# Kernel tuning notes

Hardware: AMD Instinct MI355X
Metric: run time of the kernel (lower is better)

Reference implementation:

```python
import jax, jax.numpy as jnp
import numpy as np

N = 100000      # nodes
E = 1600000     # edges (avg degree 16)
D = 64          # in_channels == conv widths == lin width
G = 64          # graphs in batch
OUT = 10        # out_channels


def setup_inputs() -> dict:
    key = jax.random.key(0)
    ks = jax.random.split(key, 20)
    s = 0.1
    inp = {
        "x": jax.random.normal(ks[0], (N, D), jnp.float32),
        "edge_index": jax.random.randint(ks[1], (2, E), 0, N, dtype=jnp.int64),
        "batch": jnp.sort(jax.random.randint(ks[2], (N,), 0, G, dtype=jnp.int64)),
    }
    k = 3
    for i in range(3):  # 3 SAGEConv layers: lin_l (Wl, bl) on aggregated, lin_r (Wr, no bias) on root
        inp[f"c{i}_Wl"] = jax.random.normal(ks[k], (D, D), jnp.float32) * s; k += 1
        inp[f"c{i}_bl"] = jnp.zeros((D,), jnp.float32)
        inp[f"c{i}_Wr"] = jax.random.normal(ks[k], (D, D), jnp.float32) * s; k += 1
    inp["l0_W"] = jax.random.normal(ks[k], (D, D), jnp.float32) * s; k += 1
    inp["l0_b"] = jnp.zeros((D,), jnp.float32)
    inp["out_W"] = jax.random.normal(ks[k], (D, OUT), jnp.float32) * s; k += 1
    inp["out_b"] = jnp.zeros((OUT,), jnp.float32)
    return inp


def reference(x, edge_index, batch,
              c0_Wl, c0_bl, c0_Wr,
              c1_Wl, c1_bl, c1_Wr,
              c2_Wl, c2_bl, c2_Wr,
              l0_W, l0_b, out_W, out_b):
    src, dst = edge_index[0], edge_index[1]
    # in-degree of each target node (mean conv aggregation), computed once
    deg = jax.ops.segment_sum(jnp.ones((E,), x.dtype), dst, num_segments=N)
    inv_deg = (1.0 / jnp.maximum(deg, 1.0))[:, None]

    def sage(h, Wl, bl, Wr):
        # gather source features, mean-aggregate at targets, then lin_l(agg) + lin_r(h)
        agg = jax.ops.segment_sum(h[src], dst, num_segments=N) * inv_deg
        return agg @ Wl + bl + h @ Wr

    h = jax.nn.relu(sage(x, c0_Wl, c0_bl, c0_Wr))
    h = jax.nn.relu(sage(h, c1_Wl, c1_bl, c1_Wr))
    h = jax.nn.relu(sage(h, c2_Wl, c2_bl, c2_Wr))

    # global mean pool over graphs
    cnt = jax.ops.segment_sum(jnp.ones((N,), h.dtype), batch, num_segments=G)
    g = jax.ops.segment_sum(h, batch, num_segments=G) / jnp.maximum(cnt, 1.0)[:, None]

    g = jax.nn.relu(g @ l0_W + l0_b)
    return g @ out_W + out_b  # [G, OUT]
```

## Files before the change

### kernel.cpp

```cpp
#include <hip/hip_runtime.h>
#include <hip/hip_fp16.h>

#define WPB 8
#define PADK 136
#define BSH 8
#define BNODES 256
#define SC_BLOCKS 256
#define HIST_BLOCKS 256
#define HSTRIDE 512

typedef _Float16 half8 __attribute__((ext_vector_type(8)));
typedef _Float16 half4v __attribute__((ext_vector_type(4)));
typedef float floatx4 __attribute__((ext_vector_type(4)));

__global__ __launch_bounds__(256) void gnn_pre(const int* __restrict__ dst,
                                               int* __restrict__ bkt_cnt, int nbkt, int E,
                                               const int* __restrict__ batch,
                                               float* __restrict__ gcnt, int N,
                                               const float4* __restrict__ xin,
                                               ushort4* __restrict__ x16o, int n4,
                                               __half* __restrict__ x16,
                                               __half* __restrict__ hA,
                                               __half* __restrict__ hB,
                                               int* __restrict__ hist_all) {
    int tid = threadIdx.x;
    if (blockIdx.x < HIST_BLOCKS) {
        __shared__ int h[512];
        __shared__ int gb[64];
        for (int i = tid; i < nbkt; i += 256) h[i] = 0;
        if (tid < 64) gb[tid] = 0;
        __syncthreads();
        const int stride = HIST_BLOCKS * 256;
        if ((E & 3) == 0) {
            const int4* dst4 = (const int4*)dst;
            int E4 = E >> 2;
            for (int e = blockIdx.x * 256 + tid; e < E4; e += stride) {
                int4 d = dst4[e];
                atomicAdd(&h[d.x >> BSH], 1);
                atomicAdd(&h[d.y >> BSH], 1);
                atomicAdd(&h[d.z >> BSH], 1);
                atomicAdd(&h[d.w >> BSH], 1);
            }
        } else {
            for (int e = blockIdx.x * 256 + tid; e < E; e += stride)
                atomicAdd(&h[dst[e] >> BSH], 1);
        }
        for (int i = blockIdx.x * 256 + tid; i < N; i += stride)
            atomicAdd(&gb[batch[i]], 1);
        __syncthreads();
        for (int i = tid; i < nbkt; i += 256) {
            int v = h[i];
            hist_all[blockIdx.x * HSTRIDE + i] = v;
            if (v) atomicAdd(&bkt_cnt[i], v);
        }
        if (tid < 64) {
            int v = gb[tid];
            if (v) atomicAdd(&gcnt[tid], (float)v);
        }
        if (blockIdx.x == 0 && tid < 64) {
            x16[(size_t)N * 64 + tid] = __ushort_as_half((unsigned short)0);
            hA[(size_t)N * 64 + tid] = __ushort_as_half((unsigned short)0);
            hB[(size_t)N * 64 + tid] = __ushort_as_half((unsigned short)0);
        }
    } else {
        int i = (blockIdx.x - HIST_BLOCKS) * 256 + tid;
        if (i < n4) {
            float4 f = xin[i];
            ushort4 o;
            o.x = __half_as_ushort(__float2half(f.x));
            o.y = __half_as_ushort(__float2half(f.y));
            o.z = __half_as_ushort(__float2half(f.z));
            o.w = __half_as_ushort(__float2half(f.w));
            x16o[i] = o;
        }
    }
}

__global__ void gnn_bkt_scan(const int* __restrict__ bkt_cnt, int* __restrict__ bkt_base,
                             int* __restrict__ row_ptr, int nbkt, int N) {
    int lane = threadIdx.x;
    int carry = 0;
    for (int base = 0; base < nbkt; base += 64) {
        int idx = base + lane;
        int v = (idx < nbkt) ? bkt_cnt[idx] : 0;
        int x = v;
#pragma unroll
        for (int off = 1; off < 64; off <<= 1) {
            int y = __shfl_up(x, off);
            if (lane >= off) x += y;
        }
        if (idx < nbkt) bkt_base[idx] = carry + (x - v);
        carry += __shfl(x, 63);
    }
    if (lane == 0) {
        bkt_base[nbkt] = carry;
        row_ptr[N] = carry;
    }
}

__global__ __launch_bounds__(256) void gnn_scan2(const int* __restrict__ hist_all,
                                                 const int* __restrict__ bkt_base,
                                                 int* __restrict__ blk_base_all, int nbkt) {
    int b = blockIdx.x;
    int t = threadIdx.x, lane = t & 63, wv = t >> 6;
    __shared__ int wsum[4];
    int v = hist_all[t * HSTRIDE + b];
    int x = v;
#pragma unroll
    for (int off = 1; off < 64; off <<= 1) {
        int y = __shfl_up(x, off);
        if (lane >= off) x += y;
    }
    if (lane == 63) wsum[wv] = x;
    __syncthreads();
    int wexcl = 0;
    for (int w = 0; w < wv; w++) wexcl += wsum[w];
    blk_base_all[t * HSTRIDE + b] = bkt_base[b] + wexcl + (x - v);
}

__global__ __launch_bounds__(256) void gnn_bkt_scatter(const int* __restrict__ src,
                                                       const int* __restrict__ dst,
                                                       const int* __restrict__ blk_base_all,
                                                       unsigned int* __restrict__ pairs,
                                                       int E, int nbkt) {
    __shared__ int cur[512];
    int tid = threadIdx.x;
    for (int i = tid; i < nbkt; i += 256) cur[i] = blk_base_all[blockIdx.x * HSTRIDE + i];
    __syncthreads();
    const int stride = SC_BLOCKS * 256;
    if ((E & 3) == 0) {
        const int4* dst4 = (const int4*)dst;
        const int4* src4 = (const int4*)src;
        int E4 = E >> 2;
        for (int e = blockIdx.x * 256 + tid; e < E4; e += stride) {
            int4 d = dst4[e];
            int4 s = src4[e];
            int p0 = atomicAdd(&cur[d.x >> BSH], 1);
            pairs[p0] = (unsigned int)s.x | ((unsigned int)(d.x & (BNODES - 1)) << 24);
            int p1 = atomicAdd(&cur[d.y >> BSH], 1);
            pairs[p1] = (unsigned int)s.y | ((unsigned int)(d.y & (BNODES - 1)) << 24);
            int p2 = atomicAdd(&cur[d.z >> BSH], 1);
            pairs[p2] = (unsigned int)s.z | ((unsigned int)(d.z & (BNODES - 1)) << 24);
            int p3 = atomicAdd(&cur[d.w >> BSH], 1);
            pairs[p3] = (unsigned int)s.w | ((unsigned int)(d.w & (BNODES - 1)) << 24);
        }
    } else {
        for (int e = blockIdx.x * 256 + tid; e < E; e += stride) {
            int d = dst[e];
            int b = d >> BSH;
            int p = atomicAdd(&cur[b], 1);
            pairs[p] = (unsigned int)src[e] | ((unsigned int)(d & (BNODES - 1)) << 24);
        }
    }
}

__global__ __launch_bounds__(256) void gnn_bkt_csr(const unsigned int* __restrict__ pairs,
                                                   const int* __restrict__ bkt_base,
                                                   int* __restrict__ row_ptr,
                                                   float* __restrict__ inv_deg,
                                                   int* __restrict__ csr_src, int N) {
    __shared__ int hist[BNODES];
    __shared__ int excl[BNODES];
    __shared__ int cur[BNODES];
    int b = blockIdx.x;
    int base = bkt_base[b];
    int cnt = bkt_base[b + 1] - base;
    int nd0 = b << BSH;
    int tid = threadIdx.x;
    hist[tid] = 0;
    __syncthreads();
    {
        int a0 = (4 - (base & 3)) & 3;
        a0 = min(a0, cnt);
        for (int i = tid; i < a0; i += 256) atomicAdd(&hist[pairs[base + i] >> 24], 1);
        int vcnt = (cnt - a0) >> 2;
        const uint4* p4 = (const uint4*)(pairs + base + a0);
        for (int i = tid; i < vcnt; i += 256) {
            uint4 u = p4[i];
            atomicAdd(&hist[u.x >> 24], 1);
            atomicAdd(&hist[u.y >> 24], 1);
            atomicAdd(&hist[u.z >> 24], 1);
            atomicAdd(&hist[u.w >> 24], 1);
        }
        for (int i = a0 + (vcnt << 2) + tid; i < cnt; i += 256)
            atomicAdd(&hist[pairs[base + i] >> 24], 1);
    }
    __syncthreads();
    if (tid < 64) {
        int carry = 0;
#pragma unroll
        for (int c = 0; c < BNODES; c += 64) {
            int v = hist[c + tid];
            int x = v;
#pragma unroll
            for (int off = 1; off < 64; off <<= 1) {
                int y = __shfl_up(x, off);
                if (tid >= off) x += y;
            }
            excl[c + tid] = carry + (x - v);
            carry += __shfl(x, 63);
        }
    }
    __syncthreads();
    {
        int node = nd0 + tid;
        if (node < N) {
            row_ptr[node] = base + excl[tid];
            int d = hist[tid];
            inv_deg[node] = 1.0f / (float)(d > 1 ? d : 1);
        }
        cur[tid] = excl[tid];
    }
    __syncthreads();
    {
        int a0 = (4 - (base & 3)) & 3;
        a0 = min(a0, cnt);
        for (int i = tid; i < a0; i += 256) {
            unsigned int u = pairs[base + i];
            int pos = atomicAdd(&cur[u >> 24], 1);
            csr_src[base + pos] = (int)(u & 0xFFFFFFu);
        }
        int vcnt = (cnt - a0) >> 2;
        const uint4* p4 = (const uint4*)(pairs + base + a0);
        for (int i = tid; i < vcnt; i += 256) {
            uint4 u = p4[i];
            int pos0 = atomicAdd(&cur[u.x >> 24], 1);
            csr_src[base + pos0] = (int)(u.x & 0xFFFFFFu);
            int pos1 = atomicAdd(&cur[u.y >> 24], 1);
            csr_src[base + pos1] = (int)(u.y & 0xFFFFFFu);
            int pos2 = atomicAdd(&cur[u.z >> 24], 1);
            csr_src[base + pos2] = (int)(u.z & 0xFFFFFFu);
            int pos3 = atomicAdd(&cur[u.w >> 24], 1);
            csr_src[base + pos3] = (int)(u.w & 0xFFFFFFu);
        }
        for (int i = a0 + (vcnt << 2) + tid; i < cnt; i += 256) {
            unsigned int u = pairs[base + i];
            int pos = atomicAdd(&cur[u >> 24], 1);
            csr_src[base + pos] = (int)(u & 0xFFFFFFu);
        }
    }
}

#define LOAD4(eReg, c0, vArr)                                  \
    _Pragma("unroll") for (int c_ = 0; c_ < 4; c_++) {         \
        int sj_ = __shfl(eReg, (c0) + c_ * 4 + quad);          \
        vArr[c_] = hin4v[(size_t)sj_ * 16 + m16];              \
    }
#define ACC4(vArr, accum)                                      \
    _Pragma("unroll") for (int c_ = 0; c_ < 4; c_++) {         \
        accum.x += (float)vArr[c_][0];                         \
        accum.y += (float)vArr[c_][1];                         \
        accum.z += (float)vArr[c_][2];                         \
        accum.w += (float)vArr[c_][3];                         \
    }

__global__ __launch_bounds__(512, 4) void gnn_sage(const __half* __restrict__ hin,
                                                   __half* __restrict__ hout,
                                                   const int* __restrict__ row_ptr,
                                                   const int* __restrict__ csr_src,
                                                   const float* __restrict__ inv_deg,
                                                   const float* __restrict__ Wl,
                                                   const float* __restrict__ bl,
                                                   const float* __restrict__ Wr, int n) {
    __shared__ _Float16 w_lds[64 * PADK];
    __shared__ _Float16 in_lds[WPB][16 * PADK];
    int tid = threadIdx.x, lane = tid & 63, wv = tid >> 6;
    for (int i = tid; i < 64 * 64; i += 512) {
        int k = i >> 6, nn = i & 63;
        w_lds[nn * PADK + k] = (_Float16)Wl[i];
        w_lds[nn * PADK + 64 + k] = (_Float16)Wr[i];
    }
    __syncthreads();
    int ngroups = (n + 15) >> 4;
    int g = blockIdx.x * WPB + wv;
    if (g >= ngroups) return;
    int m16 = lane & 15, quad = lane >> 4;
    int hf = lane >> 5, col = lane & 31;
    float bias[4];
#pragma unroll
    for (int nt = 0; nt < 4; nt++) bias[nt] = bl[nt * 16 + m16];
    _Float16* my_in = in_lds[wv];
    const unsigned* hin32 = (const unsigned*)hin;
    const half4v* hin4v = (const half4v*)hin;
    int nd0 = g << 4;
    int nclamp = n - 1 - nd0;
    int idx = nd0 + lane;
    int rr = (lane <= 16) ? row_ptr[min(idx, n)] : 0;
    float ig = (lane < 16) ? inv_deg[min(idx, n - 1)] : 0.0f;

#pragma unroll
    for (int jp = 0; jp < 8; jp++) {
        int j2 = jp << 1;
        int nd = nd0 + min(j2 + hf, nclamp);
        unsigned u = hin32[(size_t)nd * 32 + col];
        ((unsigned*)(my_in + (j2 + hf) * PADK + 64))[col] = u;
    }

    int ef[16];
#pragma unroll
    for (int j = 0; j < 16; j++) {
        int jj = min(j, nclamp);
        int s0 = __shfl(rr, jj), s1 = __shfl(rr, jj + 1);
        int cb = min(64, s1 - s0);
        ef[j] = (lane < cb) ? csr_src[s0 + lane] : n;
    }

#pragma unroll
    for (int jp = 0; jp < 8; jp++) {
        int j2 = jp << 1;
        int jjA = min(j2, nclamp), jjB = min(j2 + 1, nclamp);
        int s0A = __shfl(rr, jjA), s1A = __shfl(rr, jjA + 1);
        int s0B = __shfl(rr, jjB), s1B = __shfl(rr, jjB + 1);
        float idgA = __shfl(ig, jjA), idgB = __shfl(ig, jjB);
        int cbA = min(64, s1A - s0A), cbB = min(64, s1B - s0B);
        floatx4 accA = {0.f, 0.f, 0.f, 0.f};
        floatx4 accB = {0.f, 0.f, 0.f, 0.f};
        {
            half4v vA[4], vB[4];
            LOAD4(ef[j2], 0, vA);
            LOAD4(ef[j2 + 1], 0, vB);
            ACC4(vA, accA);
            ACC4(vB, accB);
        }
        if (cbA > 16) {
            half4v v0[4];
            LOAD4(ef[j2], 16, v0);
            ACC4(v0, accA);
            if (cbA > 32) { half4v v1[4]; LOAD4(ef[j2], 32, v1); ACC4(v1, accA); }
            if (cbA > 48) { half4v v2[4]; LOAD4(ef[j2], 48, v2); ACC4(v2, accA); }
        }
        if (cbB > 16) {
            half4v v0[4];
            LOAD4(ef[j2 + 1], 16, v0);
            ACC4(v0, accB);
            if (cbB > 32) { half4v v1[4]; LOAD4(ef[j2 + 1], 32, v1); ACC4(v1, accB); }
            if (cbB > 48) { half4v v2[4]; LOAD4(ef[j2 + 1], 48, v2); ACC4(v2, accB); }
        }
        for (int base_ = s0A + 64; base_ < s1A; base_ += 64) {
            int cb = min(64, s1A - base_);
            int ei = (lane < cb) ? csr_src[base_ + lane] : n;
            for (int i0 = 0; i0 < cb; i0 += 16) {
                half4v vt[4];
                LOAD4(ei, i0, vt);
                ACC4(vt, accA);
            }
        }
        for (int base_ = s0B + 64; base_ < s1B; base_ += 64) {
            int cb = min(64, s1B - base_);
            int ei = (lane < cb) ? csr_src[base_ + lane] : n;
            for (int i0 = 0; i0 < cb; i0 += 16) {
                half4v vt[4];
                LOAD4(ei, i0, vt);
                ACC4(vt, accB);
            }
        }
        accA.x += __shfl_xor(accA.x, 16); accA.y += __shfl_xor(accA.y, 16);
        accA.z += __shfl_xor(accA.z, 16); accA.w += __shfl_xor(accA.w, 16);
        accA.x += __shfl_xor(accA.x, 32); accA.y += __shfl_xor(accA.y, 32);
        accA.z += __shfl_xor(accA.z, 32); accA.w += __shfl_xor(accA.w, 32);
        accB.x += __shfl_xor(accB.x, 16); accB.y += __shfl_xor(accB.y, 16);
        accB.z += __shfl_xor(accB.z, 16); accB.w += __shfl_xor(accB.w, 16);
        accB.x += __shfl_xor(accB.x, 32); accB.y += __shfl_xor(accB.y, 32);
        accB.z += __shfl_xor(accB.z, 32); accB.w += __shfl_xor(accB.w, 32);
        if (quad == 0) {
            half4v hw;
            hw[0] = (_Float16)(accA.x * idgA);
            hw[1] = (_Float16)(accA.y * idgA);
            hw[2] = (_Float16)(accA.z * idgA);
            hw[3] = (_Float16)(accA.w * idgA);
            *(half4v*)(my_in + j2 * PADK + m16 * 4) = hw;
        } else if (quad == 1) {
            half4v hw;
            hw[0] = (_Float16)(accB.x * idgB);
            hw[1] = (_Float16)(accB.y * idgB);
            hw[2] = (_Float16)(accB.z * idgB);
            hw[3] = (_Float16)(accB.w * idgB);
            *(half4v*)(my_in + (j2 + 1) * PADK + m16 * 4) = hw;
        }
    }
    half8 afrag[4];
    const _Float16* abase = my_in + m16 * PADK + quad * 8;
#pragma unroll
    for (int ks = 0; ks < 4; ks++) afrag[ks] = *(const half8*)(abase + ks * 32);
    floatx4 accv[4];
#pragma unroll
    for (int nt = 0; nt < 4; nt++) {
        accv[nt].x = 0.f; accv[nt].y = 0.f; accv[nt].z = 0.f; accv[nt].w = 0.f;
    }
#pragma unroll
    for (int nt = 0; nt < 4; nt++) {
        const _Float16* bbase = w_lds + (nt * 16 + m16) * PADK + quad * 8;
#pragma unroll
        for (int ks = 0; ks < 4; ks++) {
            half8 bfrag = *(const half8*)(bbase + ks * 32);
            accv[nt] = __builtin_amdgcn_mfma_f32_16x16x32_f16(afrag[ks], bfrag, accv[nt], 0, 0, 0);
        }
    }
#pragma unroll
    for (int nt = 0; nt < 4; nt++) {
#pragma unroll
        for (int r = 0; r < 4; r++) {
            int node = nd0 + quad * 4 + r;
            if (node < n) {
                float v = fmaxf(accv[nt][r] + bias[nt], 0.0f);
                hout[(size_t)node * 64 + nt * 16 + m16] = __float2half(v);
            }
        }
    }
}

__global__ __launch_bounds__(512, 4) void gnn_sage_pool(const __half* __restrict__ hin,
                                                        const int* __restrict__ row_ptr,
                                                        const int* __restrict__ csr_src,
                                                        const float* __restrict__ inv_deg,
                                                        const float* __restrict__ Wl,
                                                        const float* __restrict__ bl,
                                                        const float* __restrict__ Wr,
                                                        const int* __restrict__ batch,
                                                        float* __restrict__ gsum, int n) {
    __shared__ _Float16 w_lds[64 * PADK];
    __shared__ _Float16 in_lds[WPB][16 * PADK];
    int tid = threadIdx.x, lane = tid & 63, wv = tid >> 6;
    for (int i = tid; i < 64 * 64; i += 512) {
        int k = i >> 6, nn = i & 63;
        w_lds[nn * PADK + k] = (_Float16)Wl[i];
        w_lds[nn * PADK + 64 + k] = (_Float16)Wr[i];
    }
    __syncthreads();
    int ngroups = (n + 15) >> 4;
    int g = blockIdx.x * WPB + wv;
    if (g >= ngroups) return;
    int m16 = lane & 15, quad = lane >> 4;
    int hf = lane >> 5, col = lane & 31;
    float bias[4];
#pragma unroll
    for (int nt = 0; nt < 4; nt++) bias[nt] = bl[nt * 16 + m16];
    _Float16* my_in = in_lds[wv];
    const unsigned* hin32 = (const unsigned*)hin;
    const half4v* hin4v = (const half4v*)hin;
    int nd0 = g << 4;
    int nclamp = n - 1 - nd0;
    int idx = nd0 + lane;
    int rr = (lane <= 16) ? row_ptr[min(idx, n)] : 0;
    float ig = (lane < 16) ? inv_deg[min(idx, n - 1)] : 0.0f;

#pragma unroll
    for (int jp = 0; jp < 8; jp++) {
        int j2 = jp << 1;
        int nd = nd0 + min(j2 + hf, nclamp);
        unsigned u = hin32[(size_t)nd * 32 + col];
        ((unsigned*)(my_in + (j2 + hf) * PADK + 64))[col] = u;
    }

    int ef[16];
#pragma unroll
    for (int j = 0; j < 16; j++) {
        int jj = min(j, nclamp);
        int s0 = __shfl(rr, jj), s1 = __shfl(rr, jj + 1);
        int cb = min(64, s1 - s0);
        ef[j] = (lane < cb) ? csr_src[s0 + lane] : n;
    }

#pragma unroll
    for (int jp = 0; jp < 8; jp++) {
        int j2 = jp << 1;
        int jjA = min(j2, nclamp), jjB = min(j2 + 1, nclamp);
        int s0A = __shfl(rr, jjA), s1A = __shfl(rr, jjA + 1);
        int s0B = __shfl(rr, jjB), s1B = __shfl(rr, jjB + 1);
        float idgA = __shfl(ig, jjA), idgB = __shfl(ig, jjB);
        int cbA = min(64, s1A - s0A), cbB = min(64, s1B - s0B);
        floatx4 accA = {0.f, 0.f, 0.f, 0.f};
        floatx4 accB = {0.f, 0.f, 0.f, 0.f};
        {
            half4v vA[4], vB[4];
            LOAD4(ef[j2], 0, vA);
            LOAD4(ef[j2 + 1], 0, vB);
            ACC4(vA, accA);
            ACC4(vB, accB);
        }
        if (cbA > 16) {
            half4v v0[4];
            LOAD4(ef[j2], 16, v0);
            ACC4(v0, accA);
            if (cbA > 32) { half4v v1[4]; LOAD4(ef[j2], 32, v1); ACC4(v1, accA); }
            if (cbA > 48) { half4v v2[4]; LOAD4(ef[j2], 48, v2); ACC4(v2, accA); }
        }
        if (cbB > 16) {
            half4v v0[4];
            LOAD4(ef[j2 + 1], 16, v0);
            ACC4(v0, accB);
            if (cbB > 32) { half4v v1[4]; LOAD4(ef[j2 + 1], 32, v1); ACC4(v1, accB); }
            if (cbB > 48) { half4v v2[4]; LOAD4(ef[j2 + 1], 48, v2); ACC4(v2, accB); }
        }
        for (int base_ = s0A + 64; base_ < s1A; base_ += 64) {
            int cb = min(64, s1A - base_);
            int ei = (lane < cb) ? csr_src[base_ + lane] : n;
            for (int i0 = 0; i0 < cb; i0 += 16) {
                half4v vt[4];
                LOAD4(ei, i0, vt);
                ACC4(vt, accA);
            }
        }
        for (int base_ = s0B + 64; base_ < s1B; base_ += 64) {
            int cb = min(64, s1B - base_);
            int ei = (lane < cb) ? csr_src[base_ + lane] : n;
            for (int i0 = 0; i0 < cb; i0 += 16) {
                half4v vt[4];
                LOAD4(ei, i0, vt);
                ACC4(vt, accB);
            }
        }
        accA.x += __shfl_xor(accA.x, 16); accA.y += __shfl_xor(accA.y, 16);
        accA.z += __shfl_xor(accA.z, 16); accA.w += __shfl_xor(accA.w, 16);
        accA.x += __shfl_xor(accA.x, 32); accA.y += __shfl_xor(accA.y, 32);
        accA.z += __shfl_xor(accA.z, 32); accA.w += __shfl_xor(accA.w, 32);
        accB.x += __shfl_xor(accB.x, 16); accB.y += __shfl_xor(accB.y, 16);
        accB.z += __shfl_xor(accB.z, 16); accB.w += __shfl_xor(accB.w, 16);
        accB.x += __shfl_xor(accB.x, 32); accB.y += __shfl_xor(accB.y, 32);
        accB.z += __shfl_xor(accB.z, 32); accB.w += __shfl_xor(accB.w, 32);
        if (quad == 0) {
            half4v hw;
            hw[0] = (_Float16)(accA.x * idgA);
            hw[1] = (_Float16)(accA.y * idgA);
            hw[2] = (_Float16)(accA.z * idgA);
            hw[3] = (_Float16)(accA.w * idgA);
            *(half4v*)(my_in + j2 * PADK + m16 * 4) = hw;
        } else if (quad == 1) {
            half4v hw;
            hw[0] = (_Float16)(accB.x * idgB);
            hw[1] = (_Float16)(accB.y * idgB);
            hw[2] = (_Float16)(accB.z * idgB);
            hw[3] = (_Float16)(accB.w * idgB);
            *(half4v*)(my_in + (j2 + 1) * PADK + m16 * 4) = hw;
        }
    }
    half8 afrag[4];
    const _Float16* abase = my_in + m16 * PADK + quad * 8;
#pragma unroll
    for (int ks = 0; ks < 4; ks++) afrag[ks] = *(const half8*)(abase + ks * 32);
    floatx4 accv[4];
#pragma unroll
    for (int nt = 0; nt < 4; nt++) {
        accv[nt].x = 0.f; accv[nt].y = 0.f; accv[nt].z = 0.f; accv[nt].w = 0.f;
    }
#pragma unroll
    for (int nt = 0; nt < 4; nt++) {
        const _Float16* bbase = w_lds + (nt * 16 + m16) * PADK + quad * 8;
#pragma unroll
        for (int ks = 0; ks < 4; ks++) {
            half8 bfrag = *(const half8*)(bbase + ks * 32);
            accv[nt] = __builtin_amdgcn_mfma_f32_16x16x32_f16(afrag[ks], bfrag, accv[nt], 0, 0, 0);
        }
    }
    int bFirst = batch[nd0];
    int bLast = batch[min(nd0 + 15, n - 1)];
    if (bFirst == bLast && nd0 + 15 < n) {
#pragma unroll
        for (int nt = 0; nt < 4; nt++) {
            float s = fmaxf(accv[nt][0] + bias[nt], 0.0f) + fmaxf(accv[nt][1] + bias[nt], 0.0f) +
                      fmaxf(accv[nt][2] + bias[nt], 0.0f) + fmaxf(accv[nt][3] + bias[nt], 0.0f);
            s += __shfl_xor(s, 16);
            s += __shfl_xor(s, 32);
            if (quad == 0) atomicAdd(&gsum[bFirst * 64 + nt * 16 + m16], s);
        }
    } else {
#pragma unroll
        for (int nt = 0; nt < 4; nt++) {
#pragma unroll
            for (int r = 0; r < 4; r++) {
                int node = nd0 + quad * 4 + r;
                if (node < n) {
                    int bg = batch[node];
                    float v = fmaxf(accv[nt][r] + bias[nt], 0.0f);
                    atomicAdd(&gsum[bg * 64 + nt * 16 + m16], v);
                }
            }
        }
    }
}

__global__ __launch_bounds__(1024) void gnn_head(const float* __restrict__ gsum,
                                                 const float* __restrict__ gcnt,
                                                 const float* __restrict__ l0W,
                                                 const float* __restrict__ l0b,
                                                 const float* __restrict__ outW,
                                                 const float* __restrict__ outb,
                                                 float* __restrict__ out, int G, int OUT) {
    __shared__ float gm[64 * 64];
    __shared__ float t2[64 * 64];
    int tid = threadIdx.x;
    for (int i = tid; i < G * 64; i += 1024) {
        int r = i >> 6;
        gm[i] = gsum[i] / fmaxf(gcnt[r], 1.0f);
    }
    __syncthreads();
    for (int i = tid; i < G * 64; i += 1024) {
        int r = i >> 6, c = i & 63;
        float s = l0b[c];
#pragma unroll 8
        for (int k = 0; k < 64; k++) s += gm[(r << 6) + k] * l0W[(k << 6) + c];
        t2[i] = fmaxf(s, 0.0f);
    }
    __syncthreads();
    for (int i = tid; i < G * OUT; i += 1024) {
        int r = i / OUT, c = i - r * OUT;
        float s = outb[c];
#pragma unroll 8
        for (int k = 0; k < 64; k++) s += t2[(r << 6) + k] * outW[k * OUT + c];
        out[i] = s;
    }
}

extern "C" void kernel_launch(void* const* d_in, const int* in_sizes, int n_in,
                              void* d_out, int out_size, void* d_ws, size_t ws_size,
                              hipStream_t stream) {
    const float* x = (const float*)d_in[0];
    const int* ei = (const int*)d_in[1];
    const int* batch = (const int*)d_in[2];
    const float* Wl[3] = {(const float*)d_in[3], (const float*)d_in[6], (const float*)d_in[9]};
    const float* bl[3] = {(const float*)d_in[4], (const float*)d_in[7], (const float*)d_in[10]};
    const float* Wr[3] = {(const float*)d_in[5], (const float*)d_in[8], (const float*)d_in[11]};
    const float* l0W = (const float*)d_in[12];
    const float* l0b = (const float*)d_in[13];
    const float* outW = (const float*)d_in[14];
    const float* outb = (const float*)d_in[15];

    int N = in_sizes[2];
    int E = in_sizes[1] / 2;
    int OUT = 10;
    int G = out_size / OUT;
    const int* src = ei;
    const int* dst = ei + E;
    int NBKT = (N + BNODES - 1) >> BSH;

    char* ws = (char*)d_ws;
    size_t off = 0;
    auto alloc = [&](size_t b) -> char* {
        char* p = ws + off;
        off = (off + b + 255) & ~(size_t)255;
        return p;
    };
    int* row_ptr = (int*)alloc((size_t)(N + 1) * 4);
    int* csr_src = (int*)alloc((size_t)E * 4);
    float* inv_deg = (float*)alloc((size_t)N * 4);
    size_t zoff = off;
    int* bkt_cnt = (int*)alloc((size_t)NBKT * 4);
    float* gcnt = (float*)alloc((size_t)G * 4);
    float* gsum = (float*)alloc((size_t)G * 64 * 4);
    size_t zlen = off - zoff;
    int* bkt_base = (int*)alloc((size_t)(NBKT + 1) * 4);
    int* hist_all = (int*)alloc((size_t)HIST_BLOCKS * HSTRIDE * 4);
    int* blk_base_all = (int*)alloc((size_t)HIST_BLOCKS * HSTRIDE * 4);
    unsigned int* pairs = (unsigned int*)alloc((size_t)E * 4);
    __half* x16 = (__half*)alloc((size_t)(N + 1) * 64 * 2);
    __half* hA = (__half*)alloc((size_t)(N + 1) * 64 * 2);
    __half* hB = (__half*)alloc((size_t)(N + 1) * 64 * 2);

    hipMemsetAsync(ws + zoff, 0, zlen, stream);

    int n4 = N * 64 / 4;
    int pre_blocks = HIST_BLOCKS + (n4 + 255) / 256;
    gnn_pre<<<pre_blocks, 256, 0, stream>>>(dst, bkt_cnt, NBKT, E, batch, gcnt, N,
                                            (const float4*)x, (ushort4*)x16, n4,
                                            x16, hA, hB, hist_all);
    gnn_bkt_scan<<<1, 64, 0, stream>>>(bkt_cnt, bkt_base, row_ptr, NBKT, N);
    gnn_scan2<<<NBKT, 256, 0, stream>>>(hist_all, bkt_base, blk_base_all, NBKT);
    gnn_bkt_scatter<<<SC_BLOCKS, 256, 0, stream>>>(src, dst, blk_base_all, pairs, E, NBKT);
    gnn_bkt_csr<<<NBKT, 256, 0, stream>>>(pairs, bkt_base, row_ptr, inv_deg, csr_src, N);

    int ngroups = (N + 15) >> 4;
    int sage_blocks = (ngroups + WPB - 1) / WPB;
    gnn_sage<<<sage_blocks, 512, 0, stream>>>(x16, hA, row_ptr, csr_src, inv_deg,
                                              Wl[0], bl[0], Wr[0], N);
    gnn_sage<<<sage_blocks, 512, 0, stream>>>(hA, hB, row_ptr, csr_src, inv_deg,
                                              Wl[1], bl[1], Wr[1], N);
    gnn_sage_pool<<<sage_blocks, 512, 0, stream>>>(hB, row_ptr, csr_src, inv_deg,
                                                   Wl[2], bl[2], Wr[2], batch, gsum, N);

    gnn_head<<<1, 1024, 0, stream>>>(gsum, gcnt, l0W, l0b, outW, outb, (float*)d_out, G, OUT);
}
```

Before: 293.5 us.

## Split neighbor gather across two waves per 16-node tile before MFMA

Each 16-node tile's mean-aggregation gather is now split across two waves of 8 nodes each, instead of one wave handling all 16. A block barrier follows, and then half the waves run the MFMA projection and write the output (or do the pooling atomics). The first 32 edges per node are now loaded unconditionally, and the launch bounds ask for higher occupancy. The aim is more concurrent memory-latency hiding in the irregular gather, at the cost of an extra __syncthreads, idle waves during the MFMA phase, and tighter register limits.

```diff
diff --git a/kernel.cpp b/kernel.cpp
--- a/kernel.cpp
+++ b/kernel.cpp
@@ -2,6 +2,7 @@
 #include <hip/hip_fp16.h>
 
 #define WPB 8
+#define TPB 4
 #define PADK 136
 #define BSH 8
 #define BNODES 256
@@ -254,7 +255,101 @@
         accum.w += (float)vArr[c_][3];                         \
     }
 
-__global__ __launch_bounds__(512, 4) void gnn_sage(const __half* __restrict__ hin,
+#define SAGE_GATHER_BODY                                                        \
+    int idxl = r0 + lane;                                                       \
+    int rr = (lane <= 8) ? row_ptr[min(idxl, n)] : 0;                           \
+    float ig = (lane < 8) ? inv_deg[min(idxl, n - 1)] : 0.0f;                   \
+    _Pragma("unroll")                                                           \
+    for (int jp = 0; jp < 4; jp++) {         \
+        int j2 = jp << 1;                                                       \
+        int nd = min(r0 + j2 + hf, n);                                          \
+        unsigned u = hin32[(size_t)nd * 32 + col];                              \
+        ((unsigned*)(my_in + (lr0 + j2 + hf) * PADK + 64))[col] = u;            \
+    }                                                                           \
+    int ef[8];                                                                  \
+    _Pragma("unroll")                                                           \
+    for (int j = 0; j < 8; j++) {                                               \
+        int s0 = __shfl(rr, j), s1 = __shfl(rr, j + 1);                         \
+        int cb = min(64, s1 - s0);                                              \
+        ef[j] = (lane < cb) ? csr_src[s0 + lane] : n;                           \
+    }                                                                           \
+    _Pragma("unroll")                                                           \
+    for (int jp = 0; jp < 4; jp++) {                                            \
+        int j2 = jp << 1;                                                       \
+        int s0A = __shfl(rr, j2), s1A = __shfl(rr, j2 + 1);                     \
+        int s1B = __shfl(rr, j2 + 2);                                           \
+        int s0B = s1A;                                                          \
+        float idgA = __shfl(ig, j2), idgB = __shfl(ig, j2 + 1);                 \
+        int cbA = min(64, s1A - s0A), cbB = min(64, s1B - s0B);                 \
+        floatx4 accA = {0.f, 0.f, 0.f, 0.f};                                    \
+        floatx4 accB = {0.f, 0.f, 0.f, 0.f};                                    \
+        {                                                                       \
+            half4v vA[4], vB[4];                                                \
+            LOAD4(ef[j2], 0, vA);                                               \
+            LOAD4(ef[j2 + 1], 0, vB);                                           \
+            ACC4(vA, accA);                                                     \
+            ACC4(vB, accB);                                                     \
+            LOAD4(ef[j2], 16, vA);                    \
+            LOAD4(ef[j2 + 1], 16, vB);                                          \
+            ACC4(vA, accA);                                                     \
+            ACC4(vB, accB);                                                     \
+        }                                                                       \
+        if (cbA > 32) {                                           \
+            half4v v0[4];                                                       \
+            LOAD4(ef[j2], 32, v0);                                              \
+            ACC4(v0, accA);                                                     \
+            if (cbA > 48) { half4v v1[4]; LOAD4(ef[j2], 48, v1); ACC4(v1, accA); } \
+        }                                                                       \
+        if (cbB > 32) {                                                         \
+            half4v v0[4];                                                       \
+            LOAD4(ef[j2 + 1], 32, v0);                                          \
+            ACC4(v0, accB);                                                     \
+            if (cbB > 48) { half4v v1[4]; LOAD4(ef[j2 + 1], 48, v1); ACC4(v1, accB); } \
+        }                                                                       \
+        for (int base_ = s0A + 64; base_ < s1A; base_ += 64) {                  \
+            int cb = min(64, s1A - base_);                                      \
+            int ei = (lane < cb) ? csr_src[base_ + lane] : n;                   \
+            for (int i0 = 0; i0 < cb; i0 += 16) {                               \
+                half4v vt[4];                                                   \
+                LOAD4(ei, i0, vt);                                              \
+                ACC4(vt, accA);                                                 \
+            }                                                                   \
+        }                                                                       \
+        for (int base_ = s0B + 64; base_ < s1B; base_ += 64) {                  \
+            int cb = min(64, s1B - base_);                                      \
+            int ei = (lane < cb) ? csr_src[base_ + lane] : n;                   \
+            for (int i0 = 0; i0 < cb; i0 += 16) {                               \
+                half4v vt[4];                                                   \
+                LOAD4(ei, i0, vt);                                              \
+                ACC4(vt, accB);                                                 \
+            }                                                                   \
+        }                                                                       \
+        accA.x += __shfl_xor(accA.x, 16); accA.y += __shfl_xor(accA.y, 16);     \
+        accA.z += __shfl_xor(accA.z, 16); accA.w += __shfl_xor(accA.w, 16);     \
+        accA.x += __shfl_xor(accA.x, 32); accA.y += __shfl_xor(accA.y, 32);     \
+        accA.z += __shfl_xor(accA.z, 32); accA.w += __shfl_xor(accA.w, 32);     \
+        accB.x += __shfl_xor(accB.x, 16); accB.y += __shfl_xor(accB.y, 16);     \
+        accB.z += __shfl_xor(accB.z, 16); accB.w += __shfl_xor(accB.w, 16);     \
+        accB.x += __shfl_xor(accB.x, 32); accB.y += __shfl_xor(accB.y, 32);     \
+        accB.z += __shfl_xor(accB.z, 32); accB.w += __shfl_xor(accB.w, 32);     \
+        if (quad == 0) {                                                        \
+            half4v hw;                                                          \
+            hw[0] = (_Float16)(accA.x * idgA);                                  \
+            hw[1] = (_Float16)(accA.y * idgA);                                  \
+            hw[2] = (_Float16)(accA.z * idgA);                                  \
+            hw[3] = (_Float16)(accA.w * idgA);                                  \
+            *(half4v*)(my_in + (lr0 + j2) * PADK + m16 * 4) = hw;               \
+        } else if (quad == 1) {                                                 \
+            half4v hw;                                                          \
+            hw[0] = (_Float16)(accB.x * idgB);                                  \
+            hw[1] = (_Float16)(accB.y * idgB);                                  \
+            hw[2] = (_Float16)(accB.z * idgB);                                  \
+            hw[3] = (_Float16)(accB.w * idgB);                                  \
+            *(half4v*)(my_in + (lr0 + j2 + 1) * PADK + m16 * 4) = hw;           \
+        }                                                                       \
+    }
+
+__global__ __launch_bounds__(512, 8) void gnn_sage(const __half* __restrict__ hin,
                                                    __half* __restrict__ hout,
                                                    const int* __restrict__ row_ptr,
                                                    const int* __restrict__ csr_src,
@@ -263,8 +358,8 @@
                                                    const float* __restrict__ bl,
                                                    const float* __restrict__ Wr, int n) {
     __shared__ _Float16 w_lds[64 * PADK];
-    __shared__ _Float16 in_lds[WPB][16 * PADK];
-    int tid = threadIdx.x, lane = tid & 63, wv = tid >> 6;
+    __shared__ _Float16 in_lds[TPB][16 * PADK];
+    int tid = threadIdx.x, lane = tid & 63, wvid = tid >> 6;
     for (int i = tid; i < 64 * 64; i += 512) {
         int k = i >> 6, nn = i & 63;
         w_lds[nn * PADK + k] = (_Float16)Wl[i];
@@ -272,144 +367,62 @@
     }
     __syncthreads();
     int ngroups = (n + 15) >> 4;
-    int g = blockIdx.x * WPB + wv;
-    if (g >= ngroups) return;
     int m16 = lane & 15, quad = lane >> 4;
     int hf = lane >> 5, col = lane & 31;
-    float bias[4];
-#pragma unroll
-    for (int nt = 0; nt < 4; nt++) bias[nt] = bl[nt * 16 + m16];
-    _Float16* my_in = in_lds[wv];
     const unsigned* hin32 = (const unsigned*)hin;
     const half4v* hin4v = (const half4v*)hin;
-    int nd0 = g << 4;
-    int nclamp = n - 1 - nd0;
-    int idx = nd0 + lane;
-    int rr = (lane <= 16) ? row_ptr[min(idx, n)] : 0;
-    float ig = (lane < 16) ? inv_deg[min(idx, n - 1)] : 0.0f;
-
-#pragma unroll
-    for (int jp = 0; jp < 8; jp++) {
-        int j2 = jp << 1;
-        int nd = nd0 + min(j2 + hf, nclamp);
-        unsigned u = hin32[(size_t)nd * 32 + col];
-        ((unsigned*)(my_in + (j2 + hf) * PADK + 64))[col] = u;
-    }
-
-    int ef[16];
-#pragma unroll
-    for (int j = 0; j < 16; j++) {
-        int jj = min(j, nclamp);
-        int s0 = __shfl(rr, jj), s1 = __shfl(rr, jj + 1);
-        int cb = min(64, s1 - s0);
-        ef[j] = (lane < cb) ? csr_src[s0 + lane] : n;
-    }
-
-#pragma unroll
-    for (int jp = 0; jp < 8; jp++) {
-        int j2 = jp << 1;
-        int jjA = min(j2, nclamp), jjB = min(j2 + 1, nclamp);
-        int s0A = __shfl(rr, jjA), s1A = __shfl(rr, jjA + 1);
-        int s0B = __shfl(rr, jjB), s1B = __shfl(rr, jjB + 1);
-        float idgA = __shfl(ig, jjA), idgB = __shfl(ig, jjB);
-        int cbA = min(64, s1A - s0A), cbB = min(64, s1B - s0B);
-        floatx4 accA = {0.f, 0.f, 0.f, 0.f};
-        floatx4 accB = {0.f, 0.f, 0.f, 0.f};
-        {
-            half4v vA[4], vB[4];
-            LOAD4(ef[j2], 0, vA);
-            LOAD4(ef[j2 + 1], 0, vB);
-            ACC4(vA, accA);
-            ACC4(vB, accB);
-        }
-        if (cbA > 16) {
-            half4v v0[4];
-            LOAD4(ef[j2], 16, v0);
-            ACC4(v0, accA);
-            if (cbA > 32) { half4v v1[4]; LOAD4(ef[j2], 32, v1); ACC4(v1, accA); }
-            if (cbA > 48) { half4v v2[4]; LOAD4(ef[j2], 48, v2); ACC4(v2, accA); }
-        }
-        if (cbB > 16) {
-            half4v v0[4];
-            LOAD4(ef[j2 + 1], 16, v0);
-            ACC4(v0, accB);
-            if (cbB > 32) { half4v v1[4]; LOAD4(ef[j2 + 1], 32, v1); ACC4(v1, accB); }
-            if (cbB > 48) { half4v v2[4]; LOAD4(ef[j2 + 1], 48, v2); ACC4(v2, accB); }
-        }
-        for (int base_ = s0A + 64; base_ < s1A; base_ += 64) {
-            int cb = min(64, s1A - base_);
-            int ei = (lane < cb) ? csr_src[base_ + lane] : n;
-            for (int i0 = 0; i0 < cb; i0 += 16) {
-                half4v vt[4];
-                LOAD4(ei, i0, vt);
-                ACC4(vt, accA);
+    {
+        int tg = wvid >> 1, half = wvid & 1;
+        int g = blockIdx.x * TPB + tg;
+        if (g < ngroups) {
+            _Float16* my_in = in_lds[tg];
+            int nd0 = g << 4;
+            int lr0 = half << 3;
+            int r0 = nd0 + lr0;
+            SAGE_GATHER_BODY
+        }
+    }
+    __syncthreads();
+    int gm = blockIdx.x * TPB + wvid;
+    if (wvid < TPB && gm < ngroups) {
+        _Float16* my_in = in_lds[wvid];
+        int nd0 = gm << 4;
+        float bias[4];
+#pragma unroll
+        for (int nt = 0; nt < 4; nt++) bias[nt] = bl[nt * 16 + m16];
+        half8 afrag[4];
+        const _Float16* abase = my_in + m16 * PADK + quad * 8;
+#pragma unroll
+        for (int ks = 0; ks < 4; ks++) afrag[ks] = *(const half8*)(abase + ks * 32);
+        floatx4 accv[4];
+#pragma unroll
+        for (int nt = 0; nt < 4; nt++) {
+            accv[nt].x = 0.f; accv[nt].y = 0.f; accv[nt].z = 0.f; accv[nt].w = 0.f;
+        }
+#pragma unroll
+        for (int nt = 0; nt < 4; nt++) {
+            const _Float16* bbase = w_lds + (nt * 16 + m16) * PADK + quad * 8;
+#pragma unroll
+            for (int ks = 0; ks < 4; ks++) {
+                half8 bfrag = *(const half8*)(bbase + ks * 32);
+                accv[nt] = __builtin_amdgcn_mfma_f32_16x16x32_f16(afrag[ks], bfrag, accv[nt], 0, 0, 0);
             }
         }
-        for (int base_ = s0B + 64; base_ < s1B; base_ += 64) {
-            int cb = min(64, s1B - base_);
-            int ei = (lane < cb) ? csr_src[base_ + lane] : n;
-            for (int i0 = 0; i0 < cb; i0 += 16) {
-                half4v vt[4];
-                LOAD4(ei, i0, vt);
-                ACC4(vt, accB);
+#pragma unroll
+        for (int nt = 0; nt < 4; nt++) {
+#pragma unroll
+            for (int r = 0; r < 4; r++) {
+                int node = nd0 + quad * 4 + r;
+                if (node < n) {
+                    float v = fmaxf(accv[nt][r] + bias[nt], 0.0f);
+                    hout[(size_t)node * 64 + nt * 16 + m16] = __float2half(v);
+                }
             }
         }
-        accA.x += __shfl_xor(accA.x, 16); accA.y += __shfl_xor(accA.y, 16);
-        accA.z += __shfl_xor(accA.z, 16); accA.w += __shfl_xor(accA.w, 16);
-        accA.x += __shfl_xor(accA.x, 32); accA.y += __shfl_xor(accA.y, 32);
-        accA.z += __shfl_xor(accA.z, 32); accA.w += __shfl_xor(accA.w, 32);
-        accB.x += __shfl_xor(accB.x, 16); accB.y += __shfl_xor(accB.y, 16);
-        accB.z += __shfl_xor(accB.z, 16); accB.w += __shfl_xor(accB.w, 16);
-        accB.x += __shfl_xor(accB.x, 32); accB.y += __shfl_xor(accB.y, 32);
-        accB.z += __shfl_xor(accB.z, 32); accB.w += __shfl_xor(accB.w, 32);
-        if (quad == 0) {
-            half4v hw;
-            hw[0] = (_Float16)(accA.x * idgA);
-            hw[1] = (_Float16)(accA.y * idgA);
-            hw[2] = (_Float16)(accA.z * idgA);
-            hw[3] = (_Float16)(accA.w * idgA);
-            *(half4v*)(my_in + j2 * PADK + m16 * 4) = hw;
-        } else if (quad == 1) {
-            half4v hw;
-            hw[0] = (_Float16)(accB.x * idgB);
-            hw[1] = (_Float16)(accB.y * idgB);
-            hw[2] = (_Float16)(accB.z * idgB);
-            hw[3] = (_Float16)(accB.w * idgB);
-            *(half4v*)(my_in + (j2 + 1) * PADK + m16 * 4) = hw;
-        }
-    }
-    half8 afrag[4];
-    const _Float16* abase = my_in + m16 * PADK + quad * 8;
-#pragma unroll
-    for (int ks = 0; ks < 4; ks++) afrag[ks] = *(const half8*)(abase + ks * 32);
-    floatx4 accv[4];
-#pragma unroll
-    for (int nt = 0; nt < 4; nt++) {
-        accv[nt].x = 0.f; accv[nt].y = 0.f; accv[nt].z = 0.f; accv[nt].w = 0.f;
-    }
-#pragma unroll
-    for (int nt = 0; nt < 4; nt++) {
-        const _Float16* bbase = w_lds + (nt * 16 + m16) * PADK + quad * 8;
-#pragma unroll
-        for (int ks = 0; ks < 4; ks++) {
-            half8 bfrag = *(const half8*)(bbase + ks * 32);
-            accv[nt] = __builtin_amdgcn_mfma_f32_16x16x32_f16(afrag[ks], bfrag, accv[nt], 0, 0, 0);
-        }
-    }
-#pragma unroll
-    for (int nt = 0; nt < 4; nt++) {
-#pragma unroll
-        for (int r = 0; r < 4; r++) {
-            int node = nd0 + quad * 4 + r;
-            if (node < n) {
-                float v = fmaxf(accv[nt][r] + bias[nt], 0.0f);
-                hout[(size_t)node * 64 + nt * 16 + m16] = __float2half(v);
-            }
-        }
-    }
-}
-
-__global__ __launch_bounds__(512, 4) void gnn_sage_pool(const __half* __restrict__ hin,
+    }
+}
+
+__global__ __launch_bounds__(512, 8) void gnn_sage_pool(const __half* __restrict__ hin,
                                                         const int* __restrict__ row_ptr,
                                                         const int* __restrict__ csr_src,
                                                         const float* __restrict__ inv_deg,
@@ -419,8 +432,8 @@
                                                         const int* __restrict__ batch,
                                                         float* __restrict__ gsum, int n) {
     __shared__ _Float16 w_lds[64 * PADK];
-    __shared__ _Float16 in_lds[WPB][16 * PADK];
-    int tid = threadIdx.x, lane = tid & 63, wv = tid >> 6;
+    __shared__ _Float16 in_lds[TPB][16 * PADK];
+    int tid = threadIdx.x, lane = tid & 63, wvid = tid >> 6;
     for (int i = tid; i < 64 * 64; i += 512) {
         int k = i >> 6, nn = i & 63;
         w_lds[nn * PADK + k] = (_Float16)Wl[i];
@@ -428,151 +441,69 @@
     }
     __syncthreads();
     int ngroups = (n + 15) >> 4;
-    int g = blockIdx.x * WPB + wv;
-    if (g >= ngroups) return;
     int m16 = lane & 15, quad = lane >> 4;
     int hf = lane >> 5, col = lane & 31;
-    float bias[4];
-#pragma unroll
-    for (int nt = 0; nt < 4; nt++) bias[nt] = bl[nt * 16 + m16];
-    _Float16* my_in = in_lds[wv];
     const unsigned* hin32 = (const unsigned*)hin;
     const half4v* hin4v = (const half4v*)hin;
-    int nd0 = g << 4;
-    int nclamp = n - 1 - nd0;
-    int idx = nd0 + lane;
-    int rr = (lane <= 16) ? row_ptr[min(idx, n)] : 0;
-    float ig = (lane < 16) ? inv_deg[min(idx, n - 1)] : 0.0f;
-
-#pragma unroll
-    for (int jp = 0; jp < 8; jp++) {
-        int j2 = jp << 1;
-        int nd = nd0 + min(j2 + hf, nclamp);
-        unsigned u = hin32[(size_t)nd * 32 + col];
-        ((unsigned*)(my_in + (j2 + hf) * PADK + 64))[col] = u;
-    }
-
-    int ef[16];
-#pragma unroll
-    for (int j = 0; j < 16; j++) {
-        int jj = min(j, nclamp);
-        int s0 = __shfl(rr, jj), s1 = __shfl(rr, jj + 1);
-        int cb = min(64, s1 - s0);
-        ef[j] = (lane < cb) ? csr_src[s0 + lane] : n;
-    }
-
-#pragma unroll
-    for (int jp = 0; jp < 8; jp++) {
-        int j2 = jp << 1;
-        int jjA = min(j2, nclamp), jjB = min(j2 + 1, nclamp);
-        int s0A = __shfl(rr, jjA), s1A = __shfl(rr, jjA + 1);
-        int s0B = __shfl(rr, jjB), s1B = __shfl(rr, jjB + 1);
-        float idgA = __shfl(ig, jjA), idgB = __shfl(ig, jjB);
-        int cbA = min(64, s1A - s0A), cbB = min(64, s1B - s0B);
-        floatx4 accA = {0.f, 0.f, 0.f, 0.f};
-        floatx4 accB = {0.f, 0.f, 0.f, 0.f};
-        {
-            half4v vA[4], vB[4];
-            LOAD4(ef[j2], 0, vA);
-            LOAD4(ef[j2 + 1], 0, vB);
-            ACC4(vA, accA);
-            ACC4(vB, accB);
-        }
-        if (cbA > 16) {
-            half4v v0[4];
-            LOAD4(ef[j2], 16, v0);
-            ACC4(v0, accA);
-            if (cbA > 32) { half4v v1[4]; LOAD4(ef[j2], 32, v1); ACC4(v1, accA); }
-            if (cbA > 48) { half4v v2[4]; LOAD4(ef[j2], 48, v2); ACC4(v2, accA); }
-        }
-        if (cbB > 16) {
-            half4v v0[4];
-            LOAD4(ef[j2 + 1], 16, v0);
-            ACC4(v0, accB);
-            if (cbB > 32) { half4v v1[4]; LOAD4(ef[j2 + 1], 32, v1); ACC4(v1, accB); }
-            if (cbB > 48) { half4v v2[4]; LOAD4(ef[j2 + 1], 48, v2); ACC4(v2, accB); }
-        }
-        for (int base_ = s0A + 64; base_ < s1A; base_ += 64) {
-            int cb = min(64, s1A - base_);
-            int ei = (lane < cb) ? csr_src[base_ + lane] : n;
-            for (int i0 = 0; i0 < cb; i0 += 16) {
-                half4v vt[4];
-                LOAD4(ei, i0, vt);
-                ACC4(vt, accA);
+    {
+        int tg = wvid >> 1, half = wvid & 1;
+        int g = blockIdx.x * TPB + tg;
+        if (g < ngroups) {
+            _Float16* my_in = in_lds[tg];
+            int nd0 = g << 4;
+            int lr0 = half << 3;
+            int r0 = nd0 + lr0;
+            SAGE_GATHER_BODY
+        }
+    }
+    __syncthreads();
+    int gm = blockIdx.x * TPB + wvid;
+    if (wvid < TPB && gm < ngroups) {
+        _Float16* my_in = in_lds[wvid];
+        int nd0 = gm << 4;
+        float bias[4];
+#pragma unroll
+        for (int nt = 0; nt < 4; nt++) bias[nt] = bl[nt * 16 + m16];
+        half8 afrag[4];
+        const _Float16* abase = my_in + m16 * PADK + quad * 8;
+#pragma unroll
+        for (int ks = 0; ks < 4; ks++) afrag[ks] = *(const half8*)(abase + ks * 32);
+        floatx4 accv[4];
+#pragma unroll
+        for (int nt = 0; nt < 4; nt++) {
+            accv[nt].x = 0.f; accv[nt].y = 0.f; accv[nt].z = 0.f; accv[nt].w = 0.f;
+        }
+#pragma unroll
+        for (int nt = 0; nt < 4; nt++) {
+            const _Float16* bbase = w_lds + (nt * 16 + m16) * PADK + quad * 8;
+#pragma unroll
+            for (int ks = 0; ks < 4; ks++) {
+                half8 bfrag = *(const half8*)(bbase + ks * 32);
+                accv[nt] = __builtin_amdgcn_mfma_f32_16x16x32_f16(afrag[ks], bfrag, accv[nt], 0, 0, 0);
             }
         }
-        for (int base_ = s0B + 64; base_ < s1B; base_ += 64) {
-            int cb = min(64, s1B - base_);
-            int ei = (lane < cb) ? csr_src[base_ + lane] : n;
-            for (int i0 = 0; i0 < cb; i0 += 16) {
-                half4v vt[4];
-                LOAD4(ei, i0, vt);
-                ACC4(vt, accB);
+        int bFirst = batch[nd0];
+        int bLast = batch[min(nd0 + 15, n - 1)];
+        if (bFirst == bLast && nd0 + 15 < n) {
+#pragma unroll
+            for (int nt = 0; nt < 4; nt++) {
+                float s = fmaxf(accv[nt][0] + bias[nt], 0.0f) + fmaxf(accv[nt][1] + bias[nt], 0.0f) +
+                          fmaxf(accv[nt][2] + bias[nt], 0.0f) + fmaxf(accv[nt][3] + bias[nt], 0.0f);
+                s += __shfl_xor(s, 16);
+                s += __shfl_xor(s, 32);
+                if (quad == 0) atomicAdd(&gsum[bFirst * 64 + nt * 16 + m16], s);
             }
-        }
-        accA.x += __shfl_xor(accA.x, 16); accA.y += __shfl_xor(accA.y, 16);
-        accA.z += __shfl_xor(accA.z, 16); accA.w += __shfl_xor(accA.w, 16);
-        accA.x += __shfl_xor(accA.x, 32); accA.y += __shfl_xor(accA.y, 32);
-        accA.z += __shfl_xor(accA.z, 32); accA.w += __shfl_xor(accA.w, 32);
-        accB.x += __shfl_xor(accB.x, 16); accB.y += __shfl_xor(accB.y, 16);
-        accB.z += __shfl_xor(accB.z, 16); accB.w += __shfl_xor(accB.w, 16);
-        accB.x += __shfl_xor(accB.x, 32); accB.y += __shfl_xor(accB.y, 32);
-        accB.z += __shfl_xor(accB.z, 32); accB.w += __shfl_xor(accB.w, 32);
-        if (quad == 0) {
-            half4v hw;
-            hw[0] = (_Float16)(accA.x * idgA);
-            hw[1] = (_Float16)(accA.y * idgA);
-            hw[2] = (_Float16)(accA.z * idgA);
-            hw[3] = (_Float16)(accA.w * idgA);
-            *(half4v*)(my_in + j2 * PADK + m16 * 4) = hw;
-        } else if (quad == 1) {
-            half4v hw;
-            hw[0] = (_Float16)(accB.x * idgB);
-            hw[1] = (_Float16)(accB.y * idgB);
-            hw[2] = (_Float16)(accB.z * idgB);
-            hw[3] = (_Float16)(accB.w * idgB);
-            *(half4v*)(my_in + (j2 + 1) * PADK + m16 * 4) = hw;
-        }
-    }
-    half8 afrag[4];
-    const _Float16* abase = my_in + m16 * PADK + quad * 8;
-#pragma unroll
-    for (int ks = 0; ks < 4; ks++) afrag[ks] = *(const half8*)(abase + ks * 32);
-    floatx4 accv[4];
-#pragma unroll
-    for (int nt = 0; nt < 4; nt++) {
-        accv[nt].x = 0.f; accv[nt].y = 0.f; accv[nt].z = 0.f; accv[nt].w = 0.f;
-    }
-#pragma unroll
-    for (int nt = 0; nt < 4; nt++) {
-        const _Float16* bbase = w_lds + (nt * 16 + m16) * PADK + quad * 8;
-#pragma unroll
-        for (int ks = 0; ks < 4; ks++) {
-            half8 bfrag = *(const half8*)(bbase + ks * 32);
-            accv[nt] = __builtin_amdgcn_mfma_f32_16x16x32_f16(afrag[ks], bfrag, accv[nt], 0, 0, 0);
-        }
-    }
-    int bFirst = batch[nd0];
-    int bLast = batch[min(nd0 + 15, n - 1)];
-    if (bFirst == bLast && nd0 + 15 < n) {
-#pragma unroll
-        for (int nt = 0; nt < 4; nt++) {
-            float s = fmaxf(accv[nt][0] + bias[nt], 0.0f) + fmaxf(accv[nt][1] + bias[nt], 0.0f) +
-                      fmaxf(accv[nt][2] + bias[nt], 0.0f) + fmaxf(accv[nt][3] + bias[nt], 0.0f);
-            s += __shfl_xor(s, 16);
-            s += __shfl_xor(s, 32);
-            if (quad == 0) atomicAdd(&gsum[bFirst * 64 + nt * 16 + m16], s);
-        }
-    } else {
-#pragma unroll
-        for (int nt = 0; nt < 4; nt++) {
-#pragma unroll
-            for (int r = 0; r < 4; r++) {
-                int node = nd0 + quad * 4 + r;
-                if (node < n) {
-                    int bg = batch[node];
-                    float v = fmaxf(accv[nt][r] + bias[nt], 0.0f);
-                    atomicAdd(&gsum[bg * 64 + nt * 16 + m16], v);
+        } else {
+#pragma unroll
+            for (int nt = 0; nt < 4; nt++) {
+#pragma unroll
+                for (int r = 0; r < 4; r++) {
+                    int node = nd0 + quad * 4 + r;
+                    if (node < n) {
+                        int bg = batch[node];
+                        float v = fmaxf(accv[nt][r] + bias[nt], 0.0f);
+                        atomicAdd(&gsum[bg * 64 + nt * 16 + m16], v);
+                    }
                 }
             }
         }
@@ -669,7 +600,7 @@
     gnn_bkt_csr<<<NBKT, 256, 0, stream>>>(pairs, bkt_base, row_ptr, inv_deg, csr_src, N);
 
     int ngroups = (N + 15) >> 4;
-    int sage_blocks = (ngroups + WPB - 1) / WPB;
+    int sage_blocks = (ngroups + TPB - 1) / TPB;
     gnn_sage<<<sage_blocks, 512, 0, stream>>>(x16, hA, row_ptr, csr_src, inv_deg,
                                               Wl[0], bl[0], Wr[0], N);
     gnn_sage<<<sage_blocks, 512, 0, stream>>>(hA, hB, row_ptr, csr_src, inv_deg,
```

Result: slower. 311.4 us (+6.1%).
